# Kernel tuning notes

Hardware: AMD Instinct MI355X
Metric: run time of the kernel (lower is better)

Reference implementation:

```python
import jax, jax.numpy as jnp
import numpy as np

B, T, IN, H, OUT, HOR = 512, 720, 6, 128, 3, 360


def _cell(xin, h, c, Wih, Whh, bih, bhh):
    # PyTorch LSTM gate order: i, f, g, o
    g = xin @ Wih.T + h @ Whh.T + bih + bhh
    i, f, gg, o = jnp.split(g, 4, axis=-1)
    c = jax.nn.sigmoid(f) * c + jax.nn.sigmoid(i) * jnp.tanh(gg)
    h = jax.nn.sigmoid(o) * jnp.tanh(c)
    return h, c


def _run_layer(x, Wih, Whh, bih, bhh, reverse):
    xs = x[:, ::-1] if reverse else x
    # hoist input projection out of the scan: (B,T,4H)
    pre = jnp.einsum('bti,gi->btg', xs, Wih) + bih + bhh
    h0 = jnp.zeros((x.shape[0], Whh.shape[1]), x.dtype)

    def step(carry, gt):
        h, c = carry
        g = gt + h @ Whh.T
        i, f, gg, o = jnp.split(g, 4, axis=-1)
        c = jax.nn.sigmoid(f) * c + jax.nn.sigmoid(i) * jnp.tanh(gg)
        h = jax.nn.sigmoid(o) * jnp.tanh(c)
        return (h, c), h

    (hT, cT), ys = jax.lax.scan(step, (h0, h0), jnp.swapaxes(pre, 0, 1))
    ys = jnp.swapaxes(ys, 0, 1)
    if reverse:
        ys = ys[:, ::-1]
    return ys, hT, cT


def reference(x, e0f_Wih, e0f_Whh, e0f_bih, e0f_bhh, e0b_Wih, e0b_Whh, e0b_bih, e0b_bhh,
              e1f_Wih, e1f_Whh, e1f_bih, e1f_bhh, e1b_Wih, e1b_Whh, e1b_bih, e1b_bhh,
              brh_W, brh_b, brc_W, brc_b,
              d0_Wih, d0_Whh, d0_bih, d0_bhh, d1_Wih, d1_Whh, d1_bih, d1_bhh,
              out_W, out_b, start_token):
    b = x.shape[0]
    # bidirectional encoder, layer 0 (input_dim -> H per direction)
    y0f, h0f, c0f = _run_layer(x, e0f_Wih, e0f_Whh, e0f_bih, e0f_bhh, False)
    y0b, h0b, c0b = _run_layer(x, e0b_Wih, e0b_Whh, e0b_bih, e0b_bhh, True)
    y0 = jnp.concatenate([y0f, y0b], axis=-1)  # (B,T,2H)
    # layer 1 (2H -> H per direction); dropout inactive in eval
    _, h1f, c1f = _run_layer(y0, e1f_Wih, e1f_Whh, e1f_bih, e1f_bhh, False)
    _, h1b, c1b = _run_layer(y0, e1b_Wih, e1b_Whh, e1b_bih, e1b_bhh, True)
    # (num_layers, B, 2H): cat fwd/bwd final states per layer
    h_enc = jnp.stack([jnp.concatenate([h0f, h0b], -1), jnp.concatenate([h1f, h1b], -1)])
    c_enc = jnp.stack([jnp.concatenate([c0f, c0b], -1), jnp.concatenate([c1f, c1b], -1)])
    h_dec = h_enc @ brh_W.T + brh_b  # (2,B,H)
    c_dec = c_enc @ brc_W.T + brc_b
    xin0 = jnp.broadcast_to(start_token[0, 0], (b, start_token.shape[-1]))  # (B,3)

    def dec_step(carry, _):
        h0, c0, h1, c1, xin = carry
        h0, c0 = _cell(xin, h0, c0, d0_Wih, d0_Whh, d0_bih, d0_bhh)
        h1, c1 = _cell(h0, h1, c1, d1_Wih, d1_Whh, d1_bih, d1_bhh)
        pred = h1 @ out_W.T + out_b
        return (h0, c0, h1, c1, pred), pred

    carry0 = (h_dec[0], c_dec[0], h_dec[1], c_dec[1], xin0)
    _, preds = jax.lax.scan(dec_step, carry0, None, length=HOR)  # (HOR,B,3)
    return jnp.swapaxes(preds, 0, 1)  # (B,HOR,3)


def setup_inputs() -> dict:
    ks = iter(jax.random.split(jax.random.key(0), 40))

    def p(shape, s=0.05):
        return jax.random.normal(next(ks), shape, dtype=jnp.float32) * s

    d = {"x": jax.random.normal(next(ks), (B, T, IN), dtype=jnp.float32)}
    for name, ind in (("e0f", IN), ("e0b", IN), ("e1f", 2 * H), ("e1b", 2 * H)):
        d[name + "_Wih"] = p((4 * H, ind))
        d[name + "_Whh"] = p((4 * H, H))
        d[name + "_bih"] = p((4 * H,))
        d[name + "_bhh"] = p((4 * H,))
    d["brh_W"] = p((H, 2 * H)); d["brh_b"] = p((H,))
    d["brc_W"] = p((H, 2 * H)); d["brc_b"] = p((H,))
    for name, ind in (("d0", OUT), ("d1", H)):
        d[name + "_Wih"] = p((4 * H, ind))
        d[name + "_Whh"] = p((4 * H, H))
        d[name + "_bih"] = p((4 * H,))
        d[name + "_bhh"] = p((4 * H,))
    d["out_W"] = p((OUT, H)); d["out_b"] = p((OUT,))
    d["start_token"] = p((1, 1, OUT), 0.01)
    return d
```

## Files before the change

kernel.cpp:

```cpp
#include <hip/hip_runtime.h>

typedef __attribute__((ext_vector_type(8))) short bf16x8;
typedef __attribute__((ext_vector_type(4))) float f32x4;

#define MFMA16(a,b,c) __builtin_amdgcn_mfma_f32_16x16x32_bf16((a),(b),(c),0,0,0)

#define T_SEQ  720
#define NB     512
#define HD     128
#define GD     512
#define BT     16
#define HP     136
#define HP0    168
#define YT     256
#define WLP    68
#define HORZ   360

__device__ __forceinline__ float bf2f_(unsigned short u){
  union { unsigned int i; float f; } v; v.i = ((unsigned int)u) << 16; return v.f;
}
__device__ __forceinline__ unsigned short f2bf(float f){
  union { float f; unsigned int i; } v; v.f = f;
  unsigned int r = v.i + 0x7fffu + ((v.i >> 16) & 1u);
  return (unsigned short)(r >> 16);
}
__device__ __forceinline__ float rcp_(float x){ return __builtin_amdgcn_rcpf(x); }
__device__ __forceinline__ float sigm(float x){ return rcp_(1.f + __expf(-x)); }
__device__ __forceinline__ float tanh_(float x){
  float a = fabsf(x);
  float e = __expf(-2.f * a);
  float t = (1.f - e) * rcp_(1.f + e);
  return x >= 0.f ? t : -t;
}
__device__ __forceinline__ bf16x8 cvt8(const float* p){
  bf16x8 r;
  #pragma unroll
  for (int i = 0; i < 8; ++i) r[i] = (short)f2bf(p[i]);
  return r;
}
__device__ __forceinline__ void gl_lds16(const unsigned short* g, unsigned short* l){
  __builtin_amdgcn_global_load_lds(
      (const __attribute__((address_space(1))) void*)(g),
      (__attribute__((address_space(3))) void*)(l), 16, 0, 0);
}

__global__ __launch_bounds__(512, 2)
void enc_layer0_kernel(const float* __restrict__ x,
                       const float* __restrict__ WihF, const float* __restrict__ WhhF,
                       const float* __restrict__ bihF, const float* __restrict__ bhhF,
                       const float* __restrict__ WihB, const float* __restrict__ WhhB,
                       const float* __restrict__ bihB, const float* __restrict__ bhhB,
                       unsigned short* __restrict__ y0,
                       float* __restrict__ ench, float* __restrict__ encc)
{
  __shared__ __align__(16) unsigned short h_buf[2][BT * HP0];
  const int tid  = threadIdx.x;
  const int lane = tid & 63;
  const int w    = tid >> 6;
  const int l15  = lane & 15;
  const int q    = lane >> 4;
  const int dir  = blockIdx.x >> 5;
  const int bbase = (blockIdx.x & 31) * BT;

  const float* Wih = dir ? WihB : WihF;
  const float* Whh = dir ? WhhB : WhhF;
  const float* bih = dir ? bihB : bihF;
  const float* bhh = dir ? bhhB : bhhF;

  bf16x8 bw[4][5];
  float  bias[4];
  #pragma unroll
  for (int g = 0; g < 4; ++g) {
    const int n = g * 128 + w * 16 + l15;
    #pragma unroll
    for (int kt = 0; kt < 4; ++kt)
      bw[g][kt] = cvt8(Whh + n * HD + kt * 32 + q * 8);
    bf16x8 f;
    #pragma unroll
    for (int j = 0; j < 8; ++j) {
      const int kk = q * 8 + j;
      float wv = 0.f;
      if (kk < 6)       wv = Wih[n * 6 + kk];
      else if (kk < 12) wv = Wih[n * 6 + (kk - 6)];
      f[j] = (short)f2bf(wv);
    }
    bw[g][4] = f;
    bias[g] = bih[n] + bhh[n];
  }

  int t = dir ? (T_SEQ - 1) : 0;
  const int dt = dir ? -1 : 1;
  const int xr_ = tid / 6, xk_ = tid % 6;

  float cst[4] = {0.f, 0.f, 0.f, 0.f};
  for (int i = tid; i < 2 * BT * HP0; i += 512) (&h_buf[0][0])[i] = 0;
  __syncthreads();
  float xv_cur = 0.f;
  if (tid < 96) {
    const float v0 = x[((size_t)(bbase + xr_) * T_SEQ + t) * 6 + xk_];
    const unsigned short hi = f2bf(v0);
    h_buf[0][xr_ * HP0 + 128 + xk_] = hi;
    h_buf[0][xr_ * HP0 + 134 + xk_] = f2bf(v0 - bf2f_(hi));
    xv_cur = x[((size_t)(bbase + xr_) * T_SEQ + t + dt) * 6 + xk_];
  }
  __syncthreads();

  for (int s = 0; s < T_SEQ; ++s, t += dt) {
    const int cur = s & 1, nxt = cur ^ 1;

    if (s > 0 && tid < 256) {
      const int b = tid >> 4, c8 = tid & 15;
      const bf16x8 hv = *reinterpret_cast<const bf16x8*>(&h_buf[cur][b * HP0 + c8 * 8]);
      *reinterpret_cast<bf16x8*>(y0 + ((size_t)(bbase + b) * T_SEQ + (t - dt)) * 256 + dir * HD + c8 * 8) = hv;
    }
    float xv_next = 0.f;
    if (tid < 96 && s + 2 < T_SEQ)
      xv_next = x[((size_t)(bbase + xr_) * T_SEQ + (t + 2 * dt)) * 6 + xk_];

    f32x4 acc[4];
    #pragma unroll
    for (int g = 0; g < 4; ++g) {
      acc[g][0] = bias[g]; acc[g][1] = bias[g];
      acc[g][2] = bias[g]; acc[g][3] = bias[g];
    }
    #pragma unroll
    for (int kt = 0; kt < 5; ++kt) {
      const bf16x8 af = *reinterpret_cast<const bf16x8*>(&h_buf[cur][l15 * HP0 + kt * 32 + q * 8]);
      #pragma unroll
      for (int g = 0; g < 4; ++g) acc[g] = MFMA16(af, bw[g][kt], acc[g]);
    }

    #pragma unroll
    for (int r = 0; r < 4; ++r) {
      const float i_ = acc[0][r], f_ = acc[1][r], g_ = acc[2][r], o_ = acc[3][r];
      const float c_ = sigm(f_) * cst[r] + sigm(i_) * tanh_(g_);
      cst[r] = c_;
      const float h_ = sigm(o_) * tanh_(c_);
      h_buf[nxt][(q * 4 + r) * HP0 + w * 16 + l15] = f2bf(h_);
      if (s == T_SEQ - 1) {
        const int b   = bbase + q * 4 + r;
        const int cix = w * 16 + l15;
        ench[(dir * NB + b) * HD + cix] = h_;
        encc[(dir * NB + b) * HD + cix] = c_;
      }
    }
    if (tid < 96 && s + 1 < T_SEQ) {
      const unsigned short hi = f2bf(xv_cur);
      h_buf[nxt][xr_ * HP0 + 128 + xk_] = hi;
      h_buf[nxt][xr_ * HP0 + 134 + xk_] = f2bf(xv_cur - bf2f_(hi));
    }
    xv_cur = xv_next;
    __syncthreads();
  }
  if (tid < 256) {
    const int cur = T_SEQ & 1;
    const int b = tid >> 4, c8 = tid & 15;
    const bf16x8 hv = *reinterpret_cast<const bf16x8*>(&h_buf[cur][b * HP0 + c8 * 8]);
    const int tl = dir ? 0 : (T_SEQ - 1);
    *reinterpret_cast<bf16x8*>(y0 + ((size_t)(bbase + b) * T_SEQ + tl) * 256 + dir * HD + c8 * 8) = hv;
  }
}

__global__ __launch_bounds__(512, 2)
void enc_layer1_kernel(const unsigned short* __restrict__ y0,
                       const float* __restrict__ WihF, const float* __restrict__ WhhF,
                       const float* __restrict__ bihF, const float* __restrict__ bhhF,
                       const float* __restrict__ WihB, const float* __restrict__ WhhB,
                       const float* __restrict__ bihB, const float* __restrict__ bhhB,
                       float* __restrict__ ench, float* __restrict__ encc)
{
  __shared__ __align__(16) unsigned short wlds[GD * WLP];
  __shared__ __align__(16) unsigned short ybuf[2][BT * YT];
  __shared__ __align__(16) unsigned short h_buf[2][BT * HP];

  const int tid  = threadIdx.x;
  const int lane = tid & 63;
  const int w    = tid >> 6;
  const int l15  = lane & 15;
  const int q    = lane >> 4;
  const int dir  = blockIdx.x >> 5;
  const int bbase = (blockIdx.x & 31) * BT;

  const float* Wih = dir ? WihB : WihF;
  const float* Whh = dir ? WhhB : WhhF;
  const float* bih = dir ? bihB : bihF;
  const float* bhh = dir ? bhhB : bhhF;

  for (int i = tid; i < GD * 8; i += 512) {
    const int n = i >> 3, c8 = i & 7;
    *reinterpret_cast<bf16x8*>(&wlds[n * WLP + c8 * 8]) = cvt8(Wih + n * 256 + c8 * 8);
  }

  bf16x8 bw[4][10];
  float  bias[4];
  int    nofs[4];
  #pragma unroll
  for (int g = 0; g < 4; ++g) {
    const int n = g * 128 + w * 16 + l15;
    nofs[g] = n * WLP;
    #pragma unroll
    for (int kt = 2; kt < 8; ++kt)  bw[g][kt - 2] = cvt8(Wih + n * 256 + kt * 32 + q * 8);
    #pragma unroll
    for (int kt = 8; kt < 12; ++kt) bw[g][kt - 2] = cvt8(Whh + n * HD + (kt - 8) * 32 + q * 8);
    bias[g] = bih[n] + bhh[n];
  }

  const int sb   = 2 * w + (lane >> 5);
  const int cimg = lane & 31;
  const int sig  = (cimg & 16) | ((cimg & 15) ^ (sb & 15));
  const size_t grow = (size_t)(bbase + sb) * T_SEQ * 256 + (size_t)sig * 8;
  unsigned short* ldst0 = &ybuf[0][w * 512];
  unsigned short* ldst1 = &ybuf[1][w * 512];

  int t = dir ? (T_SEQ - 1) : 0;
  const int dt = dir ? -1 : 1;

  float cst[4] = {0.f, 0.f, 0.f, 0.f};
  for (int i = tid; i < 2 * BT * HP; i += 512) (&h_buf[0][0])[i] = 0;
  gl_lds16(y0 + grow + (size_t)t * 256, ldst0);
  __syncthreads();

  for (int s = 0; s < T_SEQ; ++s, t += dt) {
    const int cur = s & 1, nxt = cur ^ 1;

    if (s + 1 < T_SEQ)
      gl_lds16(y0 + grow + (size_t)(t + dt) * 256, cur ? ldst0 : ldst1);

    f32x4 acc[4];
    #pragma unroll
    for (int g = 0; g < 4; ++g) {
      acc[g][0] = bias[g]; acc[g][1] = bias[g];
      acc[g][2] = bias[g]; acc[g][3] = bias[g];
    }
    #pragma unroll
    for (int kt = 0; kt < 2; ++kt) {
      const int swz = ((kt * 4 + q) & 15) ^ l15;
      const bf16x8 af = *reinterpret_cast<const bf16x8*>(&ybuf[cur][l15 * YT + swz * 8]);
      #pragma unroll
      for (int g = 0; g < 4; ++g) {
        const bf16x8 bl = *reinterpret_cast<const bf16x8*>(&wlds[nofs[g] + kt * 32 + q * 8]);
        acc[g] = MFMA16(af, bl, acc[g]);
      }
    }
    #pragma unroll
    for (int kt = 2; kt < 8; ++kt) {
      const int c   = kt * 4 + q;
      const int swz = (c & 16) | ((c & 15) ^ l15);
      const bf16x8 af = *reinterpret_cast<const bf16x8*>(&ybuf[cur][l15 * YT + swz * 8]);
      #pragma unroll
      for (int g = 0; g < 4; ++g) acc[g] = MFMA16(af, bw[g][kt - 2], acc[g]);
    }
    #pragma unroll
    for (int kt = 8; kt < 12; ++kt) {
      const bf16x8 af = *reinterpret_cast<const bf16x8*>(&h_buf[cur][l15 * HP + (kt - 8) * 32 + q * 8]);
      #pragma unroll
      for (int g = 0; g < 4; ++g) acc[g] = MFMA16(af, bw[g][kt - 2], acc[g]);
    }

    #pragma unroll
    for (int r = 0; r < 4; ++r) {
      const float i_ = acc[0][r], f_ = acc[1][r], g_ = acc[2][r], o_ = acc[3][r];
      const float c_ = sigm(f_) * cst[r] + sigm(i_) * tanh_(g_);
      cst[r] = c_;
      const float h_ = sigm(o_) * tanh_(c_);
      h_buf[nxt][(q * 4 + r) * HP + w * 16 + l15] = f2bf(h_);
      if (s == T_SEQ - 1) {
        const int b   = bbase + q * 4 + r;
        const int cix = w * 16 + l15;
        ench[(dir * NB + b) * HD + cix] = h_;
        encc[(dir * NB + b) * HD + cix] = c_;
      }
    }
    __syncthreads();
  }
}

__global__ void bridge_kernel(const float* __restrict__ ench0, const float* __restrict__ encc0,
                              const float* __restrict__ ench1, const float* __restrict__ encc1,
                              const float* __restrict__ brhW, const float* __restrict__ brhb,
                              const float* __restrict__ brcW, const float* __restrict__ brcb,
                              float* __restrict__ dech, float* __restrict__ decc)
{
  const int idx = blockIdx.x * 256 + threadIdx.x;
  const int sel = idx >> 17;
  const int l   = (idx >> 16) & 1;
  const int b   = (idx >> 7) & 511;
  const int j   = idx & 127;
  const float* W  = sel ? brcW : brhW;
  const float* bb = sel ? brcb : brhb;
  const float* s0 = sel ? (l ? encc1 : encc0) : (l ? ench1 : ench0);
  float a = bb[j];
  for (int k = 0; k < 128; ++k) a += W[j * 256 + k] * s0[b * 128 + k];
  for (int k = 0; k < 128; ++k) a += W[j * 256 + 128 + k] * s0[(512 + b) * 128 + k];
  float* dst = sel ? decc : dech;
  dst[(l * 512 + b) * 128 + j] = a;
}

__global__ __launch_bounds__(512, 2)
void decoder_kernel(const float* __restrict__ dech, const float* __restrict__ decc,
                    const float* __restrict__ W0ih, const float* __restrict__ W0hh,
                    const float* __restrict__ b0ih, const float* __restrict__ b0hh,
                    const float* __restrict__ W1ih, const float* __restrict__ W1hh,
                    const float* __restrict__ b1ih, const float* __restrict__ b1hh,
                    const float* __restrict__ outW, const float* __restrict__ outb,
                    const float* __restrict__ stok,
                    float* __restrict__ out)
{
  __shared__ __align__(16) unsigned short w0lds[GD * WLP];
  __shared__ __align__(16) unsigned short w1lds[GD * WLP];
  __shared__ __align__(16) unsigned short h0_buf[2][BT * HP];
  __shared__ __align__(16) unsigned short h1_buf[2][BT * HP];

  const int tid  = threadIdx.x;
  const int lane = tid & 63;
  const int w    = tid >> 6;
  const int l15  = lane & 15;
  const int q    = lane >> 4;
  const int bbase = blockIdx.x * BT;

  for (int i = tid; i < GD * 8; i += 512) {
    const int n = i >> 3, c8 = i & 7;
    *reinterpret_cast<bf16x8*>(&w0lds[n * WLP + c8 * 8]) = cvt8(W0hh + n * HD + c8 * 8);
    *reinterpret_cast<bf16x8*>(&w1lds[n * WLP + c8 * 8]) = cvt8(W1ih + n * HD + c8 * 8);
  }

  bf16x8 bw0[4][2];
  bf16x8 bw1[4][6];
  float  xw0[4][3], bias0[4], bias1[4];
  int    nofs[4];
  #pragma unroll
  for (int g = 0; g < 4; ++g) {
    const int n = g * 128 + w * 16 + l15;
    nofs[g] = n * WLP;
    #pragma unroll
    for (int kt = 2; kt < 4; ++kt) {
      bw0[g][kt - 2] = cvt8(W0hh + n * HD + kt * 32 + q * 8);
      bw1[g][kt - 2] = cvt8(W1ih + n * HD + kt * 32 + q * 8);
    }
    #pragma unroll
    for (int kt = 4; kt < 8; ++kt)
      bw1[g][kt - 2] = cvt8(W1hh + n * HD + (kt - 4) * 32 + q * 8);
    #pragma unroll
    for (int k = 0; k < 3; ++k) xw0[g][k] = W0ih[n * 3 + k];
    bias0[g] = b0ih[n] + b0hh[n];
    bias1[g] = b1ih[n] + b1hh[n];
  }

  bf16x8 owf[4];
  float outb_s = 0.f;
  {
    bf16x8 z;
    #pragma unroll
    for (int i = 0; i < 8; ++i) z[i] = 0;
    #pragma unroll
    for (int kt = 0; kt < 4; ++kt) owf[kt] = z;
    if (l15 < 3) {
      #pragma unroll
      for (int kt = 0; kt < 4; ++kt) owf[kt] = cvt8(outW + l15 * HD + kt * 32 + q * 8);
      outb_s = outb[l15];
    }
  }

  float c0[4], c1[4];
  #pragma unroll
  for (int r = 0; r < 4; ++r) {
    const int b   = bbase + q * 4 + r;
    const int cix = w * 16 + l15;
    c0[r] = decc[b * HD + cix];
    c1[r] = decc[(NB + b) * HD + cix];
  }
  for (int i = tid; i < BT * HD; i += 512) {
    const int b = i >> 7, cix = i & 127;
    h0_buf[0][b * HP + cix] = f2bf(dech[(bbase + b) * HD + cix]);
    h1_buf[0][b * HP + cix] = f2bf(dech[(NB + bbase + b) * HD + cix]);
  }
  float xr[4][3];
  {
    const float s0 = stok[0], s1 = stok[1], s2 = stok[2];
    #pragma unroll
    for (int r = 0; r < 4; ++r) { xr[r][0] = s0; xr[r][1] = s1; xr[r][2] = s2; }
  }
  __syncthreads();

  for (int s = 0; s < HORZ; ++s) {
    const int cur = s & 1, nxt = cur ^ 1;

    f32x4 acc[4];
    #pragma unroll
    for (int g = 0; g < 4; ++g)
      #pragma unroll
      for (int r = 0; r < 4; ++r)
        acc[g][r] = bias0[g] + xw0[g][0] * xr[r][0] + xw0[g][1] * xr[r][1] + xw0[g][2] * xr[r][2];
    #pragma unroll
    for (int kt = 0; kt < 2; ++kt) {
      const bf16x8 af = *reinterpret_cast<const bf16x8*>(&h0_buf[cur][l15 * HP + kt * 32 + q * 8]);
      #pragma unroll
      for (int g = 0; g < 4; ++g) {
        const bf16x8 bl = *reinterpret_cast<const bf16x8*>(&w0lds[nofs[g] + kt * 32 + q * 8]);
        acc[g] = MFMA16(af, bl, acc[g]);
      }
    }
    #pragma unroll
    for (int kt = 2; kt < 4; ++kt) {
      const bf16x8 af = *reinterpret_cast<const bf16x8*>(&h0_buf[cur][l15 * HP + kt * 32 + q * 8]);
      #pragma unroll
      for (int g = 0; g < 4; ++g) acc[g] = MFMA16(af, bw0[g][kt - 2], acc[g]);
    }
    #pragma unroll
    for (int r = 0; r < 4; ++r) {
      const float i_ = acc[0][r], f_ = acc[1][r], g_ = acc[2][r], o_ = acc[3][r];
      const float c_ = sigm(f_) * c0[r] + sigm(i_) * tanh_(g_);
      c0[r] = c_;
      const float h_ = sigm(o_) * tanh_(c_);
      h0_buf[nxt][(q * 4 + r) * HP + w * 16 + l15] = f2bf(h_);
    }
    __syncthreads();

    #pragma unroll
    for (int g = 0; g < 4; ++g) {
      acc[g][0] = bias1[g]; acc[g][1] = bias1[g];
      acc[g][2] = bias1[g]; acc[g][3] = bias1[g];
    }
    #pragma unroll
    for (int kt = 0; kt < 2; ++kt) {
      const bf16x8 af = *reinterpret_cast<const bf16x8*>(&h0_buf[nxt][l15 * HP + kt * 32 + q * 8]);
      #pragma unroll
      for (int g = 0; g < 4; ++g) {
        const bf16x8 bl = *reinterpret_cast<const bf16x8*>(&w1lds[nofs[g] + kt * 32 + q * 8]);
        acc[g] = MFMA16(af, bl, acc[g]);
      }
    }
    #pragma unroll
    for (int kt = 2; kt < 4; ++kt) {
      const bf16x8 af = *reinterpret_cast<const bf16x8*>(&h0_buf[nxt][l15 * HP + kt * 32 + q * 8]);
      #pragma unroll
      for (int g = 0; g < 4; ++g) acc[g] = MFMA16(af, bw1[g][kt - 2], acc[g]);
    }
    #pragma unroll
    for (int kt = 4; kt < 8; ++kt) {
      const bf16x8 af = *reinterpret_cast<const bf16x8*>(&h1_buf[cur][l15 * HP + (kt - 4) * 32 + q * 8]);
      #pragma unroll
      for (int g = 0; g < 4; ++g) acc[g] = MFMA16(af, bw1[g][kt - 2], acc[g]);
    }
    #pragma unroll
    for (int r = 0; r < 4; ++r) {
      const float i_ = acc[0][r], f_ = acc[1][r], g_ = acc[2][r], o_ = acc[3][r];
      const float c_ = sigm(f_) * c1[r] + sigm(i_) * tanh_(g_);
      c1[r] = c_;
      const float h_ = sigm(o_) * tanh_(c_);
      h1_buf[nxt][(q * 4 + r) * HP + w * 16 + l15] = f2bf(h_);
    }
    __syncthreads();

    f32x4 p = {0.f, 0.f, 0.f, 0.f};
    #pragma unroll
    for (int kt = 0; kt < 4; ++kt) {
      const bf16x8 af = *reinterpret_cast<const bf16x8*>(&h1_buf[nxt][l15 * HP + kt * 32 + q * 8]);
      p = MFMA16(af, owf[kt], p);
    }
    float pb[4];
    #pragma unroll
    for (int r = 0; r < 4; ++r) pb[r] = p[r] + outb_s;
    if (w == 0 && l15 < 3) {
      #pragma unroll
      for (int r = 0; r < 4; ++r)
        out[((size_t)(bbase + q * 4 + r) * HORZ + s) * 3 + l15] = pb[r];
    }
    #pragma unroll
    for (int r = 0; r < 4; ++r)
      #pragma unroll
      for (int c = 0; c < 3; ++c)
        xr[r][c] = __shfl(pb[r], (q << 4) + c, 64);
  }
}

extern "C" void kernel_launch(void* const* d_in, const int* in_sizes, int n_in,
                              void* d_out, int out_size, void* d_ws, size_t ws_size,
                              hipStream_t stream)
{
  (void)in_sizes; (void)n_in; (void)out_size; (void)ws_size;
  const float* x      = (const float*)d_in[0];
  const float* e0fWih = (const float*)d_in[1];
  const float* e0fWhh = (const float*)d_in[2];
  const float* e0fbih = (const float*)d_in[3];
  const float* e0fbhh = (const float*)d_in[4];
  const float* e0bWih = (const float*)d_in[5];
  const float* e0bWhh = (const float*)d_in[6];
  const float* e0bbih = (const float*)d_in[7];
  const float* e0bbhh = (const float*)d_in[8];
  const float* e1fWih = (const float*)d_in[9];
  const float* e1fWhh = (const float*)d_in[10];
  const float* e1fbih = (const float*)d_in[11];
  const float* e1fbhh = (const float*)d_in[12];
  const float* e1bWih = (const float*)d_in[13];
  const float* e1bWhh = (const float*)d_in[14];
  const float* e1bbih = (const float*)d_in[15];
  const float* e1bbhh = (const float*)d_in[16];
  const float* brhW   = (const float*)d_in[17];
  const float* brhb   = (const float*)d_in[18];
  const float* brcW   = (const float*)d_in[19];
  const float* brcb   = (const float*)d_in[20];
  const float* d0Wih  = (const float*)d_in[21];
  const float* d0Whh  = (const float*)d_in[22];
  const float* d0bih  = (const float*)d_in[23];
  const float* d0bhh  = (const float*)d_in[24];
  const float* d1Wih  = (const float*)d_in[25];
  const float* d1Whh  = (const float*)d_in[26];
  const float* d1bih  = (const float*)d_in[27];
  const float* d1bhh  = (const float*)d_in[28];
  const float* outW   = (const float*)d_in[29];
  const float* outb   = (const float*)d_in[30];
  const float* stok   = (const float*)d_in[31];

  char* ws = (char*)d_ws;
  unsigned short* y0 = (unsigned short*)ws;
  size_t off = (size_t)NB * T_SEQ * 256 * sizeof(unsigned short);
  const size_t blk = (size_t)2 * NB * HD * sizeof(float);
  float* ench0 = (float*)(ws + off); off += blk;
  float* encc0 = (float*)(ws + off); off += blk;
  float* ench1 = (float*)(ws + off); off += blk;
  float* encc1 = (float*)(ws + off); off += blk;
  float* dech  = (float*)(ws + off); off += blk;
  float* decc  = (float*)(ws + off); off += blk;

  enc_layer0_kernel<<<dim3(64), dim3(512), 0, stream>>>(
      x, e0fWih, e0fWhh, e0fbih, e0fbhh, e0bWih, e0bWhh, e0bbih, e0bbhh,
      y0, ench0, encc0);
  enc_layer1_kernel<<<dim3(64), dim3(512), 0, stream>>>(
      y0, e1fWih, e1fWhh, e1fbih, e1fbhh, e1bWih, e1bWhh, e1bbih, e1bbhh,
      ench1, encc1);
  bridge_kernel<<<dim3(1024), dim3(256), 0, stream>>>(
      ench0, encc0, ench1, encc1, brhW, brhb, brcW, brcb, dech, decc);
  decoder_kernel<<<dim3(32), dim3(512), 0, stream>>>(
      dech, decc, d0Wih, d0Whh, d0bih, d0bhh, d1Wih, d1Whh, d1bih, d1bhh,
      outW, outb, stok, (float*)d_out);
}
```

Before: 3.036 ms.

## Software-pipeline encoder layer1 and decoder recurrences, fold biases into MFMA init

Encoder layer 1 now uses a triple-buffered y0 stage and computes the input-projection part of step s+1 while step s's recurrent part and gates run, so the y-dependent MFMAs leave the serial chain. The decoder moves the h1-recurrent MFMAs and the output projection ahead of the layer-0 gate work, and feeds the previous prediction through an LDS stage into a bf16 MFMA instead of scalar FMAs plus shuffles. Biases seed the first MFMA accumulator, and tanh becomes a single exp+rcp form. Costs are more registers and LDS, bf16 rounding of the fed-back prediction, and a tanh that may overflow for large negative inputs.

```diff
diff --git a/kernel.cpp b/kernel.cpp
--- a/kernel.cpp
+++ b/kernel.cpp
@@ -27,10 +27,7 @@
 __device__ __forceinline__ float rcp_(float x){ return __builtin_amdgcn_rcpf(x); }
 __device__ __forceinline__ float sigm(float x){ return rcp_(1.f + __expf(-x)); }
 __device__ __forceinline__ float tanh_(float x){
-  float a = fabsf(x);
-  float e = __expf(-2.f * a);
-  float t = (1.f - e) * rcp_(1.f + e);
-  return x >= 0.f ? t : -t;
+  return __builtin_fmaf(2.f, rcp_(1.f + __expf(-2.f * x)), -1.f);
 }
 __device__ __forceinline__ bf16x8 cvt8(const float* p){
   bf16x8 r;
@@ -68,7 +65,7 @@
   const float* bhh = dir ? bhhB : bhhF;
 
   bf16x8 bw[4][5];
-  float  bias[4];
+  f32x4  bias_vec[4];
   #pragma unroll
   for (int g = 0; g < 4; ++g) {
     const int n = g * 128 + w * 16 + l15;
@@ -85,7 +82,8 @@
       f[j] = (short)f2bf(wv);
     }
     bw[g][4] = f;
-    bias[g] = bih[n] + bhh[n];
+    const float b = bih[n] + bhh[n];
+    bias_vec[g][0] = b; bias_vec[g][1] = b; bias_vec[g][2] = b; bias_vec[g][3] = b;
   }
 
   int t = dir ? (T_SEQ - 1) : 0;
@@ -119,15 +117,11 @@
 
     f32x4 acc[4];
     #pragma unroll
-    for (int g = 0; g < 4; ++g) {
-      acc[g][0] = bias[g]; acc[g][1] = bias[g];
-      acc[g][2] = bias[g]; acc[g][3] = bias[g];
-    }
-    #pragma unroll
     for (int kt = 0; kt < 5; ++kt) {
       const bf16x8 af = *reinterpret_cast<const bf16x8*>(&h_buf[cur][l15 * HP0 + kt * 32 + q * 8]);
       #pragma unroll
-      for (int g = 0; g < 4; ++g) acc[g] = MFMA16(af, bw[g][kt], acc[g]);
+      for (int g = 0; g < 4; ++g)
+        acc[g] = MFMA16(af, bw[g][kt], kt == 0 ? bias_vec[g] : acc[g]);
     }
 
     #pragma unroll
@@ -161,6 +155,64 @@
   }
 }
 
+#define ENC1_YPART(ACC, YB)                                                    \
+  {                                                                            \
+    _Pragma("unroll")                                                          \
+    for (int g = 0; g < 4; ++g) {                                              \
+      (ACC)[g][0] = bias[g]; (ACC)[g][1] = bias[g];                            \
+      (ACC)[g][2] = bias[g]; (ACC)[g][3] = bias[g];                            \
+    }                                                                          \
+    _Pragma("unroll")                                                          \
+    for (int kt = 0; kt < 2; ++kt) {                                           \
+      const int swz_ = ((kt * 4 + q) & 15) ^ l15;                              \
+      const bf16x8 af = *reinterpret_cast<const bf16x8*>(&(YB)[l15 * YT + swz_ * 8]); \
+      _Pragma("unroll")                                                        \
+      for (int g = 0; g < 4; ++g) {                                            \
+        const bf16x8 bl = *reinterpret_cast<const bf16x8*>(&wlds[nofs[g] + kt * 32 + q * 8]); \
+        (ACC)[g] = MFMA16(af, bl, (ACC)[g]);                                   \
+      }                                                                        \
+    }                                                                          \
+    _Pragma("unroll")                                                          \
+    for (int kt = 2; kt < 8; ++kt) {                                           \
+      const int c_ = kt * 4 + q;                                               \
+      const int swz_ = (c_ & 16) | ((c_ & 15) ^ l15);                          \
+      const bf16x8 af = *reinterpret_cast<const bf16x8*>(&(YB)[l15 * YT + swz_ * 8]); \
+      _Pragma("unroll")                                                        \
+      for (int g = 0; g < 4; ++g) (ACC)[g] = MFMA16(af, bw[g][kt - 2], (ACC)[g]); \
+    }                                                                          \
+  }
+
+#define ENC1_BODY(S, CUR, NXT, ACCC, ACCN)                                     \
+  {                                                                            \
+    if ((S) + 2 < T_SEQ)                                                       \
+      gl_lds16(y0 + grow + (size_t)(t + 2 * dt) * 256, b2 + w * 512);          \
+    _Pragma("unroll")                                                          \
+    for (int kt = 8; kt < 12; ++kt) {                                          \
+      const bf16x8 af = *reinterpret_cast<const bf16x8*>(&h_buf[CUR][l15 * HP + (kt - 8) * 32 + q * 8]); \
+      _Pragma("unroll")                                                        \
+      for (int g = 0; g < 4; ++g) (ACCC)[g] = MFMA16(af, bw[g][kt - 2], (ACCC)[g]); \
+    }                                                                          \
+    if ((S) + 1 < T_SEQ) ENC1_YPART(ACCN, b1)                                  \
+    _Pragma("unroll")                                                          \
+    for (int r = 0; r < 4; ++r) {                                              \
+      const float i_ = (ACCC)[0][r], f_ = (ACCC)[1][r];                        \
+      const float g_ = (ACCC)[2][r], o_ = (ACCC)[3][r];                        \
+      const float cc_ = sigm(f_) * cst[r] + sigm(i_) * tanh_(g_);              \
+      cst[r] = cc_;                                                            \
+      const float h_ = sigm(o_) * tanh_(cc_);                                  \
+      h_buf[NXT][(q * 4 + r) * HP + w * 16 + l15] = f2bf(h_);                  \
+      if ((S) == T_SEQ - 1) {                                                  \
+        const int b_ = bbase + q * 4 + r;                                      \
+        const int cix = w * 16 + l15;                                          \
+        ench[(dir * NB + b_) * HD + cix] = h_;                                 \
+        encc[(dir * NB + b_) * HD + cix] = cc_;                                \
+      }                                                                        \
+    }                                                                          \
+    { unsigned short* tmp_ = b0; b0 = b1; b1 = b2; b2 = tmp_; }                \
+    t += dt;                                                                   \
+    __syncthreads();                                                           \
+  }
+
 __global__ __launch_bounds__(512, 2)
 void enc_layer1_kernel(const unsigned short* __restrict__ y0,
                        const float* __restrict__ WihF, const float* __restrict__ WhhF,
@@ -170,7 +222,7 @@
                        float* __restrict__ ench, float* __restrict__ encc)
 {
   __shared__ __align__(16) unsigned short wlds[GD * WLP];
-  __shared__ __align__(16) unsigned short ybuf[2][BT * YT];
+  __shared__ __align__(16) unsigned short ybuf[3][BT * YT];
   __shared__ __align__(16) unsigned short h_buf[2][BT * HP];
 
   const int tid  = threadIdx.x;
@@ -209,69 +261,26 @@
   const int cimg = lane & 31;
   const int sig  = (cimg & 16) | ((cimg & 15) ^ (sb & 15));
   const size_t grow = (size_t)(bbase + sb) * T_SEQ * 256 + (size_t)sig * 8;
-  unsigned short* ldst0 = &ybuf[0][w * 512];
-  unsigned short* ldst1 = &ybuf[1][w * 512];
+  unsigned short* b0 = &ybuf[0][0];
+  unsigned short* b1 = &ybuf[1][0];
+  unsigned short* b2 = &ybuf[2][0];
 
   int t = dir ? (T_SEQ - 1) : 0;
   const int dt = dir ? -1 : 1;
 
   float cst[4] = {0.f, 0.f, 0.f, 0.f};
   for (int i = tid; i < 2 * BT * HP; i += 512) (&h_buf[0][0])[i] = 0;
-  gl_lds16(y0 + grow + (size_t)t * 256, ldst0);
+  gl_lds16(y0 + grow + (size_t)t * 256,        b0 + w * 512);
+  gl_lds16(y0 + grow + (size_t)(t + dt) * 256, b1 + w * 512);
   __syncthreads();
 
-  for (int s = 0; s < T_SEQ; ++s, t += dt) {
-    const int cur = s & 1, nxt = cur ^ 1;
-
-    if (s + 1 < T_SEQ)
-      gl_lds16(y0 + grow + (size_t)(t + dt) * 256, cur ? ldst0 : ldst1);
-
-    f32x4 acc[4];
-    #pragma unroll
-    for (int g = 0; g < 4; ++g) {
-      acc[g][0] = bias[g]; acc[g][1] = bias[g];
-      acc[g][2] = bias[g]; acc[g][3] = bias[g];
-    }
-    #pragma unroll
-    for (int kt = 0; kt < 2; ++kt) {
-      const int swz = ((kt * 4 + q) & 15) ^ l15;
-      const bf16x8 af = *reinterpret_cast<const bf16x8*>(&ybuf[cur][l15 * YT + swz * 8]);
-      #pragma unroll
-      for (int g = 0; g < 4; ++g) {
-        const bf16x8 bl = *reinterpret_cast<const bf16x8*>(&wlds[nofs[g] + kt * 32 + q * 8]);
-        acc[g] = MFMA16(af, bl, acc[g]);
-      }
-    }
-    #pragma unroll
-    for (int kt = 2; kt < 8; ++kt) {
-      const int c   = kt * 4 + q;
-      const int swz = (c & 16) | ((c & 15) ^ l15);
-      const bf16x8 af = *reinterpret_cast<const bf16x8*>(&ybuf[cur][l15 * YT + swz * 8]);
-      #pragma unroll
-      for (int g = 0; g < 4; ++g) acc[g] = MFMA16(af, bw[g][kt - 2], acc[g]);
-    }
-    #pragma unroll
-    for (int kt = 8; kt < 12; ++kt) {
-      const bf16x8 af = *reinterpret_cast<const bf16x8*>(&h_buf[cur][l15 * HP + (kt - 8) * 32 + q * 8]);
-      #pragma unroll
-      for (int g = 0; g < 4; ++g) acc[g] = MFMA16(af, bw[g][kt - 2], acc[g]);
-    }
-
-    #pragma unroll
-    for (int r = 0; r < 4; ++r) {
-      const float i_ = acc[0][r], f_ = acc[1][r], g_ = acc[2][r], o_ = acc[3][r];
-      const float c_ = sigm(f_) * cst[r] + sigm(i_) * tanh_(g_);
-      cst[r] = c_;
-      const float h_ = sigm(o_) * tanh_(c_);
-      h_buf[nxt][(q * 4 + r) * HP + w * 16 + l15] = f2bf(h_);
-      if (s == T_SEQ - 1) {
-        const int b   = bbase + q * 4 + r;
-        const int cix = w * 16 + l15;
-        ench[(dir * NB + b) * HD + cix] = h_;
-        encc[(dir * NB + b) * HD + cix] = c_;
-      }
-    }
-    __syncthreads();
+  f32x4 accP[4], accQ[4];
+  ENC1_YPART(accP, b0)
+
+  for (int m = 0; m < T_SEQ / 2; ++m) {
+    const int s0 = 2 * m;
+    ENC1_BODY(s0,     0, 1, accP, accQ)
+    ENC1_BODY(s0 + 1, 1, 0, accQ, accP)
   }
 }
 
@@ -310,6 +319,8 @@
   __shared__ __align__(16) unsigned short w1lds[GD * WLP];
   __shared__ __align__(16) unsigned short h0_buf[2][BT * HP];
   __shared__ __align__(16) unsigned short h1_buf[2][BT * HP];
+  __shared__ __align__(16) unsigned short xstage[8][BT * 8];
+  __shared__ __align__(16) unsigned short xzero[8];
 
   const int tid  = threadIdx.x;
   const int lane = tid & 63;
@@ -326,7 +337,8 @@
 
   bf16x8 bw0[4][2];
   bf16x8 bw1[4][6];
-  float  xw0[4][3], bias0[4], bias1[4];
+  bf16x8 wx0[4];
+  f32x4  bias0_vec[4], bias1_vec[4];
   int    nofs[4];
   #pragma unroll
   for (int g = 0; g < 4; ++g) {
@@ -340,10 +352,17 @@
     #pragma unroll
     for (int kt = 4; kt < 8; ++kt)
       bw1[g][kt - 2] = cvt8(W1hh + n * HD + (kt - 4) * 32 + q * 8);
-    #pragma unroll
-    for (int k = 0; k < 3; ++k) xw0[g][k] = W0ih[n * 3 + k];
-    bias0[g] = b0ih[n] + b0hh[n];
-    bias1[g] = b1ih[n] + b1hh[n];
+    bf16x8 f;
+    #pragma unroll
+    for (int j = 0; j < 8; ++j) {
+      const int kk = q * 8 + j;
+      f[j] = (short)((kk < 3) ? f2bf(W0ih[n * 3 + kk]) : 0);
+    }
+    wx0[g] = f;
+    const float b0 = b0ih[n] + b0hh[n];
+    const float b1 = b1ih[n] + b1hh[n];
+    bias0_vec[g][0] = b0; bias0_vec[g][1] = b0; bias0_vec[g][2] = b0; bias0_vec[g][3] = b0;
+    bias1_vec[g][0] = b1; bias1_vec[g][1] = b1; bias1_vec[g][2] = b1; bias1_vec[g][3] = b1;
   }
 
   bf16x8 owf[4];
@@ -374,41 +393,66 @@
     h0_buf[0][b * HP + cix] = f2bf(dech[(bbase + b) * HD + cix]);
     h1_buf[0][b * HP + cix] = f2bf(dech[(NB + bbase + b) * HD + cix]);
   }
-  float xr[4][3];
   {
-    const float s0 = stok[0], s1 = stok[1], s2 = stok[2];
-    #pragma unroll
-    for (int r = 0; r < 4; ++r) { xr[r][0] = s0; xr[r][1] = s1; xr[r][2] = s2; }
-  }
+    const int row = lane >> 2, col = lane & 3;
+    const unsigned short v = (col < 3) ? f2bf(stok[col]) : 0;
+    xstage[w][row * 8 + col] = v;
+    xstage[w][row * 8 + 4 + col] = 0;
+    if (tid < 8) xzero[tid] = 0;
+  }
+  const unsigned short* afx_ptr = (q == 0) ? &xstage[w][l15 * 8] : xzero;
   __syncthreads();
 
   for (int s = 0; s < HORZ; ++s) {
     const int cur = s & 1, nxt = cur ^ 1;
 
-    f32x4 acc[4];
-    #pragma unroll
-    for (int g = 0; g < 4; ++g)
-      #pragma unroll
-      for (int r = 0; r < 4; ++r)
-        acc[g][r] = bias0[g] + xw0[g][0] * xr[r][0] + xw0[g][1] * xr[r][1] + xw0[g][2] * xr[r][2];
+    f32x4 accC[4];
+    #pragma unroll
+    for (int kt = 4; kt < 8; ++kt) {
+      const bf16x8 af = *reinterpret_cast<const bf16x8*>(&h1_buf[cur][l15 * HP + (kt - 4) * 32 + q * 8]);
+      #pragma unroll
+      for (int g = 0; g < 4; ++g)
+        accC[g] = MFMA16(af, bw1[g][kt - 2], kt == 4 ? bias1_vec[g] : accC[g]);
+    }
+    f32x4 p = {0.f, 0.f, 0.f, 0.f};
+    #pragma unroll
+    for (int kt = 0; kt < 4; ++kt) {
+      const bf16x8 af = *reinterpret_cast<const bf16x8*>(&h1_buf[cur][l15 * HP + kt * 32 + q * 8]);
+      p = MFMA16(af, owf[kt], p);
+    }
+    f32x4 acc0[4];
     #pragma unroll
     for (int kt = 0; kt < 2; ++kt) {
       const bf16x8 af = *reinterpret_cast<const bf16x8*>(&h0_buf[cur][l15 * HP + kt * 32 + q * 8]);
       #pragma unroll
       for (int g = 0; g < 4; ++g) {
         const bf16x8 bl = *reinterpret_cast<const bf16x8*>(&w0lds[nofs[g] + kt * 32 + q * 8]);
-        acc[g] = MFMA16(af, bl, acc[g]);
+        acc0[g] = MFMA16(af, bl, kt == 0 ? bias0_vec[g] : acc0[g]);
       }
     }
     #pragma unroll
     for (int kt = 2; kt < 4; ++kt) {
       const bf16x8 af = *reinterpret_cast<const bf16x8*>(&h0_buf[cur][l15 * HP + kt * 32 + q * 8]);
       #pragma unroll
-      for (int g = 0; g < 4; ++g) acc[g] = MFMA16(af, bw0[g][kt - 2], acc[g]);
+      for (int g = 0; g < 4; ++g) acc0[g] = MFMA16(af, bw0[g][kt - 2], acc0[g]);
+    }
+    if (l15 < 3) {
+      #pragma unroll
+      for (int r = 0; r < 4; ++r) {
+        const float v = p[r] + outb_s;
+        xstage[w][(q * 4 + r) * 8 + l15] = f2bf(v);
+        if (w == 0 && s > 0)
+          out[((size_t)(bbase + q * 4 + r) * HORZ + (s - 1)) * 3 + l15] = v;
+      }
+    }
+    {
+      const bf16x8 afx = *reinterpret_cast<const bf16x8*>(afx_ptr);
+      #pragma unroll
+      for (int g = 0; g < 4; ++g) acc0[g] = MFMA16(afx, wx0[g], acc0[g]);
     }
     #pragma unroll
     for (int r = 0; r < 4; ++r) {
-      const float i_ = acc[0][r], f_ = acc[1][r], g_ = acc[2][r], o_ = acc[3][r];
+      const float i_ = acc0[0][r], f_ = acc0[1][r], g_ = acc0[2][r], o_ = acc0[3][r];
       const float c_ = sigm(f_) * c0[r] + sigm(i_) * tanh_(g_);
       c0[r] = c_;
       const float h_ = sigm(o_) * tanh_(c_);
@@ -417,60 +461,44 @@
     __syncthreads();
 
     #pragma unroll
-    for (int g = 0; g < 4; ++g) {
-      acc[g][0] = bias1[g]; acc[g][1] = bias1[g];
-      acc[g][2] = bias1[g]; acc[g][3] = bias1[g];
-    }
-    #pragma unroll
     for (int kt = 0; kt < 2; ++kt) {
       const bf16x8 af = *reinterpret_cast<const bf16x8*>(&h0_buf[nxt][l15 * HP + kt * 32 + q * 8]);
       #pragma unroll
       for (int g = 0; g < 4; ++g) {
         const bf16x8 bl = *reinterpret_cast<const bf16x8*>(&w1lds[nofs[g] + kt * 32 + q * 8]);
-        acc[g] = MFMA16(af, bl, acc[g]);
+        accC[g] = MFMA16(af, bl, accC[g]);
       }
     }
     #pragma unroll
     for (int kt = 2; kt < 4; ++kt) {
       const bf16x8 af = *reinterpret_cast<const bf16x8*>(&h0_buf[nxt][l15 * HP + kt * 32 + q * 8]);
       #pragma unroll
-      for (int g = 0; g < 4; ++g) acc[g] = MFMA16(af, bw1[g][kt - 2], acc[g]);
-    }
-    #pragma unroll
-    for (int kt = 4; kt < 8; ++kt) {
-      const bf16x8 af = *reinterpret_cast<const bf16x8*>(&h1_buf[cur][l15 * HP + (kt - 4) * 32 + q * 8]);
-      #pragma unroll
-      for (int g = 0; g < 4; ++g) acc[g] = MFMA16(af, bw1[g][kt - 2], acc[g]);
+      for (int g = 0; g < 4; ++g) accC[g] = MFMA16(af, bw1[g][kt - 2], accC[g]);
     }
     #pragma unroll
     for (int r = 0; r < 4; ++r) {
-      const float i_ = acc[0][r], f_ = acc[1][r], g_ = acc[2][r], o_ = acc[3][r];
+      const float i_ = accC[0][r], f_ = accC[1][r], g_ = accC[2][r], o_ = accC[3][r];
       const float c_ = sigm(f_) * c1[r] + sigm(i_) * tanh_(g_);
       c1[r] = c_;
       const float h_ = sigm(o_) * tanh_(c_);
       h1_buf[nxt][(q * 4 + r) * HP + w * 16 + l15] = f2bf(h_);
     }
     __syncthreads();
-
+  }
+
+  {
+    const int cur = HORZ & 1;
     f32x4 p = {0.f, 0.f, 0.f, 0.f};
     #pragma unroll
     for (int kt = 0; kt < 4; ++kt) {
-      const bf16x8 af = *reinterpret_cast<const bf16x8*>(&h1_buf[nxt][l15 * HP + kt * 32 + q * 8]);
+      const bf16x8 af = *reinterpret_cast<const bf16x8*>(&h1_buf[cur][l15 * HP + kt * 32 + q * 8]);
       p = MFMA16(af, owf[kt], p);
     }
-    float pb[4];
-    #pragma unroll
-    for (int r = 0; r < 4; ++r) pb[r] = p[r] + outb_s;
     if (w == 0 && l15 < 3) {
       #pragma unroll
       for (int r = 0; r < 4; ++r)
-        out[((size_t)(bbase + q * 4 + r) * HORZ + s) * 3 + l15] = pb[r];
-    }
-    #pragma unroll
-    for (int r = 0; r < 4; ++r)
-      #pragma unroll
-      for (int c = 0; c < 3; ++c)
-        xr[r][c] = __shfl(pb[r], (q << 4) + c, 64);
+        out[((size_t)(bbase + q * 4 + r) * HORZ + (HORZ - 1)) * 3 + l15] = p[r] + outb_s;
+    }
   }
 }
 
```

New measurement: 3.146 ms. 3.6% more time.
